# Performance work log

Measured on AMD Instinct MI355X. Metric: run time of the kernel, lower is better.

## Reference

```python
import jax, jax.numpy as jnp
import numpy as np

B, C, H, W = 16, 256, 56, 56
PH, PW = 7, 7            # partition (window) size
HEADS, DH = 8, 32        # n_heads = C // head_dim
P = PH * PW              # tokens per window = 49
GH, GW = H // PH, W // PW
G = GH * GW              # number of windows = 64
MLP = 4                  # mlp_ratio
EPS = 1e-5
SCALE = C ** (-0.5)      # note: torch code scales by feat_dim, not head_dim


def _rel_index(h, w):
    coords = np.stack(np.meshgrid(np.arange(h), np.arange(w), indexing='ij'))  # [2,h,w]
    cf = coords.reshape(2, -1)
    rel = cf[:, :, None] - cf[:, None, :]              # [2,P,P]
    rel = rel.transpose(1, 2, 0)
    rel[:, :, 0] += h - 1
    rel[:, :, 1] += w - 1
    rel[:, :, 0] *= 2 * w - 1
    return rel.sum(-1).astype(np.int32)                # [P,P]


def setup_inputs() -> dict:
    key = jax.random.key(0)
    ks = jax.random.split(key, 8)
    std = 0.02
    return {
        'x': jax.random.normal(ks[0], (B, C, H, W), jnp.float32),
        'ln1_g': jnp.ones((C,), jnp.float32),
        'ln1_b': jnp.zeros((C,), jnp.float32),
        'wqkv': jax.random.normal(ks[1], (C, 3 * C), jnp.float32) * std,
        'bqkv': jnp.zeros((3 * C,), jnp.float32),
        'wmerge': jax.random.normal(ks[2], (C, C), jnp.float32) * std,
        'bmerge': jnp.zeros((C,), jnp.float32),
        'bias_table': jax.random.normal(ks[3], ((2 * PH - 1) * (2 * PW - 1), HEADS), jnp.float32) * std,
        'ln2_g': jnp.ones((C,), jnp.float32),
        'ln2_b': jnp.zeros((C,), jnp.float32),
        'w1': jax.random.normal(ks[4], (C, MLP * C), jnp.float32) * std,
        'b1': jnp.zeros((MLP * C,), jnp.float32),
        'w2': jax.random.normal(ks[5], (MLP * C, C), jnp.float32) * std,
        'b2': jnp.zeros((C,), jnp.float32),
        'rel_idx': jnp.asarray(_rel_index(PH, PW)),
    }


def _layernorm(x, g, b):
    mu = jnp.mean(x, axis=-1, keepdims=True)
    var = jnp.var(x, axis=-1, keepdims=True)
    return (x - mu) * jax.lax.rsqrt(var + EPS) * g + b


def reference(x, ln1_g, ln1_b, wqkv, bqkv, wmerge, bmerge, bias_table,
              ln2_g, ln2_b, w1, b1, w2, b2, rel_idx):
    # --- window partition: [B,C,H,W] -> [B,G,P,C]
    xw = x.reshape(B, C, GH, PH, GW, PW).transpose(0, 2, 4, 3, 5, 1).reshape(B, G, P, C)

    # --- relative-position attention block
    y = _layernorm(xw, ln1_g, ln1_b)
    qkv = y @ wqkv + bqkv                               # [B,G,P,3C]
    q, k, v = jnp.split(qkv, 3, axis=-1)
    q = q.reshape(B, G, P, HEADS, DH)
    k = k.reshape(B, G, P, HEADS, DH) * SCALE
    v = v.reshape(B, G, P, HEADS, DH)
    scores = jnp.einsum('bgihd,bgjhd->bghij', q, k)     # [B,G,H,P,P]
    bias = bias_table[rel_idx].transpose(2, 0, 1)       # [H,P,P]
    attn = jax.nn.softmax(scores + bias[None, None], axis=-1)
    out = jnp.einsum('bghij,bgjhd->bgihd', attn, v).reshape(B, G, P, C)
    out = out @ wmerge + bmerge
    xw = xw + out

    # --- MLP block
    z = _layernorm(xw, ln2_g, ln2_b)
    z = jax.nn.gelu(z @ w1 + b1, approximate=False) @ w2 + b2
    xw = xw + z

    # --- window departition: [B,G,P,C] -> [B,C,H,W]
    xo = xw.reshape(B, GH, GW, PH, PW, C).transpose(0, 5, 1, 3, 2, 4).reshape(B, C, H, W)
    return xo
```

## Files before the change

### kernel.cpp

```cpp
#include <hip/hip_runtime.h>
#include <hip/hip_bf16.h>

#define B_      16
#define C_      256
#define H_      56
#define W_      56
#define HW_     3136
#define G_      64
#define P_      49
#define NTOK    50176
#define HEADS_  8
#define DH_     32
#define SCALE_  0.0625f
#define EPS_    1e-5f

typedef short bf16x8 __attribute__((ext_vector_type(8)));
typedef short bf16x4_t __attribute__((ext_vector_type(4)));
typedef float f32x4  __attribute__((ext_vector_type(4)));
using bf16 = __hip_bfloat16;

__device__ __forceinline__ void gload16(const void* g, void* l) {
  __builtin_amdgcn_global_load_lds((const __attribute__((address_space(1))) void*)g,
                                   (__attribute__((address_space(3))) void*)l, 16, 0, 0);
}
__device__ __forceinline__ float b2f(short s) {
  union { float f; unsigned u; } v; v.u = ((unsigned)(unsigned short)s) << 16; return v.f;
}
__device__ __forceinline__ short f2b(float f) {
  union { float f; unsigned u; } v; v.f = f;
  unsigned r = (v.u + 0x7FFFu + ((v.u >> 16) & 1u)) >> 16;
  return (short)r;
}

__global__ __launch_bounds__(256)
void prep_kernel(const float* __restrict__ wqkv, const float* __restrict__ wmerge,
                 const float* __restrict__ w1, const float* __restrict__ w2,
                 const float* __restrict__ btab, const int* __restrict__ relidx,
                 bf16* __restrict__ wqkvT, bf16* __restrict__ wmergeT,
                 bf16* __restrict__ w1T, bf16* __restrict__ w2T,
                 short* __restrict__ bt)
{
  int idx = blockIdx.x * 256 + threadIdx.x;
  if (idx < 196608) { int n = idx >> 8, k = idx & 255;
    wqkvT[idx] = __float2bfloat16(wqkv[k * 768 + n]); return; }
  idx -= 196608;
  if (idx < 65536) { int n = idx >> 8, k = idx & 255;
    wmergeT[idx] = __float2bfloat16(wmerge[k * 256 + n]); return; }
  idx -= 65536;
  if (idx < 262144) { int n = idx >> 8, k = idx & 255;
    w1T[idx] = __float2bfloat16(w1[k * 1024 + n]); return; }
  idx -= 262144;
  if (idx < 262144) { int n = idx >> 10, k = idx & 1023;
    w2T[idx] = __float2bfloat16(w2[k * 256 + n]); return; }
  idx -= 262144;
  if (idx < 32768) {
    int h = idx >> 12, rest = idx & 4095;
    int key = rest >> 6, col = rest & 63;
    int q = col >> 2, qni = col & 3;
    int query = qni * 16 + q;
    float v = 0.f;
    if (key < P_ && query < P_) v = btab[relidx[query * P_ + key] * HEADS_ + h];
    bt[idx] = f2b(v);
  }
}

__global__ __launch_bounds__(256)
void ingest_kernel(const float* __restrict__ x, const float* __restrict__ gam,
                   const float* __restrict__ bet, short* __restrict__ xtok,
                   short* __restrict__ y)
{
  __shared__ short Lt[56 * 260];
  const int h = blockIdx.x % 56, b = blockIdx.x / 56;
  const int tid = threadIdx.x;

  const float* xb = x + (size_t)b * 256 * HW_ + h * 56;
#pragma unroll
  for (int i = 0; i < 14; i++) {
    int idx = i * 256 + tid;
    int c = idx / 14, w4 = idx - c * 14;
    float4 v = *(const float4*)(xb + (size_t)c * HW_ + w4 * 4);
    Lt[(w4 * 4 + 0) * 260 + c] = f2b(v.x);
    Lt[(w4 * 4 + 1) * 260 + c] = f2b(v.y);
    Lt[(w4 * 4 + 2) * 260 + c] = f2b(v.z);
    Lt[(w4 * 4 + 3) * 260 + c] = f2b(v.w);
  }
  __syncthreads();

  const int lane = tid & 63, wv = tid >> 6;
  float4 gv = *(const float4*)(gam + lane * 4);
  float4 bv = *(const float4*)(bet + lane * 4);
  const int hdiv = h / 7, hmod = h - hdiv * 7;

  for (int t = 0; t < 14; t++) {
    int w = wv * 14 + t;
    bf16x4_t raw = *(const bf16x4_t*)&Lt[w * 260 + lane * 4];
    float f0 = b2f(raw[0]), f1 = b2f(raw[1]), f2 = b2f(raw[2]), f3 = b2f(raw[3]);
    float sum = f0 + f1 + f2 + f3;
    float sq  = f0*f0 + f1*f1 + f2*f2 + f3*f3;
#pragma unroll
    for (int off = 32; off > 0; off >>= 1) {
      sum += __shfl_xor(sum, off, 64);
      sq  += __shfl_xor(sq,  off, 64);
    }
    float mu = sum * (1.0f / 256.0f);
    float var = sq * (1.0f / 256.0f) - mu * mu;
    float rs = rsqrtf(var + EPS_);
    int wdiv = w / 7, wmod = w - wdiv * 7;
    int tok = b * HW_ + (hdiv * 8 + wdiv) * P_ + hmod * 7 + wmod;
    *(bf16x4_t*)(xtok + (size_t)tok * 256 + lane * 4) = raw;
    bf16x4_t o;
    o[0] = f2b((f0 - mu) * rs * gv.x + bv.x);
    o[1] = f2b((f1 - mu) * rs * gv.y + bv.y);
    o[2] = f2b((f2 - mu) * rs * gv.z + bv.z);
    o[3] = f2b((f3 - mu) * rs * gv.w + bv.w);
    *(bf16x4_t*)(y + (size_t)tok * 256 + lane * 4) = o;
  }
}

__global__ __launch_bounds__(256)
void ln2_kernel(const short* __restrict__ xw, const float* __restrict__ gam,
                const float* __restrict__ bet, short* __restrict__ z)
{
  const int t = blockIdx.x * 4 + (threadIdx.x >> 6);
  const int lane = threadIdx.x & 63;
  bf16x4_t raw = *(const bf16x4_t*)(xw + (size_t)t * 256 + lane * 4);
  float v[4];
#pragma unroll
  for (int j = 0; j < 4; j++) v[j] = b2f(raw[j]);
  float sum = v[0] + v[1] + v[2] + v[3];
  float sq  = v[0]*v[0] + v[1]*v[1] + v[2]*v[2] + v[3]*v[3];
#pragma unroll
  for (int off = 32; off > 0; off >>= 1) {
    sum += __shfl_xor(sum, off, 64);
    sq  += __shfl_xor(sq,  off, 64);
  }
  float mu = sum * (1.0f / 256.0f);
  float var = sq * (1.0f / 256.0f) - mu * mu;
  float rs = rsqrtf(var + EPS_);
  bf16x4_t o;
#pragma unroll
  for (int j = 0; j < 4; j++) {
    int c = lane * 4 + j;
    o[j] = f2b((v[j] - mu) * rs * gam[c] + bet[c]);
  }
  *(bf16x4_t*)(z + (size_t)t * 256 + lane * 4) = o;
}

__global__ __launch_bounds__(256)
void egress_kernel(const short* __restrict__ outtok, float* __restrict__ out)
{
  const int h = blockIdx.x % 56, b = blockIdx.x / 56;
  const int w = threadIdx.x & 63, cblk = threadIdx.x >> 6;
  const bool act = w < 56;
  const int wcl = act ? w : 55;
  const int tok = b * HW_ + ((h / 7) * 8 + wcl / 7) * P_ + (h % 7) * 7 + (wcl % 7);
  const short* src = outtok + (size_t)tok * 256 + cblk * 64;
  float* dst = out + ((size_t)b * 256 + cblk * 64) * HW_ + h * 56 + w;
#pragma unroll
  for (int j0 = 0; j0 < 64; j0 += 8) {
    bf16x8 r = *(const bf16x8*)(src + j0);
#pragma unroll
    for (int jj = 0; jj < 8; jj++)
      if (act) dst[(size_t)(j0 + jj) * HW_] = b2f(r[jj]);
  }
}

__global__ __launch_bounds__(64)
void attn_kernel(const short* __restrict__ qkv, const short* __restrict__ bt,
                 short* __restrict__ out)
{
  __shared__ short Pbuf[64 * 72];
  const int bid = blockIdx.x;
  const int h = bid & 7;
  const int t0 = (bid >> 3) * P_;
  const int lane = threadIdx.x;
  const int g = lane >> 4, q = lane & 15;

  const short* qb = qkv + (size_t)t0 * 768 + h * 32;

  bf16x8 vf[2][2];
#pragma unroll
  for (int kkt = 0; kkt < 2; kkt++)
#pragma unroll
    for (int n2 = 0; n2 < 2; n2++)
#pragma unroll
      for (int jj = 0; jj < 8; jj++) {
        int key = kkt * 32 + 8 * g + jj; key = key > 48 ? 48 : key;
        vf[kkt][n2][jj] = qb[(size_t)key * 768 + 512 + n2 * 16 + q];
      }

  bf16x8 kf[4], qf[4];
#pragma unroll
  for (int mi = 0; mi < 4; mi++) {
    int r_ = mi * 16 + q; r_ = r_ > 48 ? 48 : r_;
    kf[mi] = *(const bf16x8*)(qb + (size_t)r_ * 768 + 256 + 8 * g);
  }
#pragma unroll
  for (int ni = 0; ni < 4; ni++) {
    int r_ = ni * 16 + q; r_ = r_ > 48 ? 48 : r_;
    qf[ni] = *(const bf16x8*)(qb + (size_t)r_ * 768 + 8 * g);
  }

  f32x4 sacc[4][4] = {};
#pragma unroll
  for (int mi = 0; mi < 4; mi++)
#pragma unroll
    for (int ni = 0; ni < 4; ni++)
      sacc[mi][ni] = __builtin_amdgcn_mfma_f32_16x16x32_bf16(kf[mi], qf[ni], sacc[mi][ni], 0, 0, 0);

  float mx[4] = {-1e30f, -1e30f, -1e30f, -1e30f};
  const short* btb = bt + (size_t)(h * 64) * 64 + q * 4;
#pragma unroll
  for (int mi = 0; mi < 4; mi++)
#pragma unroll
    for (int r = 0; r < 4; r++) {
      int key = mi * 16 + 4 * g + r;
      bf16x4_t bv = *(const bf16x4_t*)(btb + key * 64);
      bool valid = key < P_;
#pragma unroll
      for (int ni = 0; ni < 4; ni++) {
        float s = valid ? fmaf(sacc[mi][ni][r], SCALE_, b2f(bv[ni])) : -1e30f;
        sacc[mi][ni][r] = s;
        mx[ni] = fmaxf(mx[ni], s);
      }
    }
#pragma unroll
  for (int ni = 0; ni < 4; ni++) {
    mx[ni] = fmaxf(mx[ni], __shfl_xor(mx[ni], 16, 64));
    mx[ni] = fmaxf(mx[ni], __shfl_xor(mx[ni], 32, 64));
  }
  float sm[4] = {0.f, 0.f, 0.f, 0.f};
#pragma unroll
  for (int mi = 0; mi < 4; mi++)
#pragma unroll
    for (int ni = 0; ni < 4; ni++)
#pragma unroll
      for (int r = 0; r < 4; r++) {
        float p = __expf(sacc[mi][ni][r] - mx[ni]);
        sacc[mi][ni][r] = p;
        sm[ni] += p;
      }
#pragma unroll
  for (int ni = 0; ni < 4; ni++) {
    sm[ni] += __shfl_xor(sm[ni], 16, 64);
    sm[ni] += __shfl_xor(sm[ni], 32, 64);
    sm[ni] = 1.0f / sm[ni];
  }
#pragma unroll
  for (int ni = 0; ni < 4; ni++)
#pragma unroll
    for (int mi = 0; mi < 4; mi++) {
      bf16x4_t pv;
#pragma unroll
      for (int r = 0; r < 4; r++) pv[r] = f2b(sacc[mi][ni][r] * sm[ni]);
      *(bf16x4_t*)&Pbuf[(ni * 16 + q) * 72 + mi * 16 + 4 * g] = pv;
    }
  __syncthreads();

  f32x4 oacc[4][2] = {};
#pragma unroll
  for (int kkt = 0; kkt < 2; kkt++) {
    bf16x8 paf[4];
#pragma unroll
    for (int qi = 0; qi < 4; qi++)
      paf[qi] = *(const bf16x8*)&Pbuf[(qi * 16 + q) * 72 + kkt * 32 + 8 * g];
#pragma unroll
    for (int qi = 0; qi < 4; qi++)
#pragma unroll
      for (int n2 = 0; n2 < 2; n2++)
        oacc[qi][n2] = __builtin_amdgcn_mfma_f32_16x16x32_bf16(paf[qi], vf[kkt][n2], oacc[qi][n2], 0, 0, 0);
  }

  short* ob = out + (size_t)t0 * 256 + h * 32;
#pragma unroll
  for (int qi = 0; qi < 4; qi++)
#pragma unroll
    for (int r = 0; r < 4; r++) {
      int query = qi * 16 + 4 * g + r;
      if (query < P_) {
#pragma unroll
        for (int n2 = 0; n2 < 2; n2++)
          ob[(size_t)query * 256 + n2 * 16 + q] = f2b(oacc[qi][n2][r]);
      }
    }
}

template<int EPI, int WN>
__global__ __launch_bounds__(128 * WN)
void gemm_kernel(const bf16* __restrict__ A, const bf16* __restrict__ Wt,
                 const float* __restrict__ bias, int N, int K,
                 bf16* __restrict__ outb, short* __restrict__ res_io)
{
  constexpr int THREADS = 128 * WN;
  constexpr int BN = 64 * WN;
  constexpr int RPP = THREADS / 4;
  constexpr int APASS = 128 / RPP;
  constexpr int BPASS = BN / RPP;
  constexpr int NLOADS = APASS + BPASS;
  __shared__ __align__(16) bf16 As[2][128 * 32];
  __shared__ __align__(16) bf16 Bs[2][BN * 32];

  const int tid = threadIdx.x;
  const int lane = tid & 63;
  const int wave = tid >> 6;
  const int wr = wave / WN, wc = wave % WN;
  const int bm = blockIdx.y * 128, bn = blockIdx.x * BN;

  f32x4 acc[4][4] = {};

  const int trow = tid >> 2;
  const int tcol = ((tid & 3) ^ ((tid >> 3) & 3)) * 8;
  const bf16* aA[APASS];
#pragma unroll
  for (int p = 0; p < APASS; p++)
    aA[p] = A + (size_t)(bm + p * RPP + trow) * K + tcol;
  const bf16* aB[BPASS];
#pragma unroll
  for (int p = 0; p < BPASS; p++)
    aB[p] = Wt + (size_t)(bn + p * RPP + trow) * K + tcol;
  const int dOff = tid * 8;

  const int kc_sw = ((lane >> 4) ^ ((lane >> 1) & 3)) * 8;
  const int l15 = lane & 15, g = lane >> 4;
  const int rA = wr * 64 + l15;
  const int rB = wc * 64 + l15;

  const int nt = K >> 5;

#pragma unroll
  for (int p = 0; p < APASS; p++) gload16(aA[p], &As[0][p * RPP * 32 + dOff]);
#pragma unroll
  for (int p = 0; p < BPASS; p++) gload16(aB[p], &Bs[0][p * RPP * 32 + dOff]);
#pragma unroll
  for (int p = 0; p < APASS; p++) gload16(aA[p] + 32, &As[1][p * RPP * 32 + dOff]);
#pragma unroll
  for (int p = 0; p < BPASS; p++) gload16(aB[p] + 32, &Bs[1][p * RPP * 32 + dOff]);

  for (int t = 0; t < nt; ++t) {
    const int cur = t & 1;
    if (t + 1 < nt) {
      if constexpr (NLOADS == 3) asm volatile("s_waitcnt vmcnt(3)" ::: "memory");
      else                       asm volatile("s_waitcnt vmcnt(4)" ::: "memory");
    } else {
      asm volatile("s_waitcnt vmcnt(0)" ::: "memory");
    }
    __builtin_amdgcn_s_barrier();

    bf16x8 af[4], bfr[4];
#pragma unroll
    for (int i = 0; i < 4; i++) {
      af[i]  = *(const bf16x8*)(&As[cur][(rA + i * 16) * 32 + kc_sw]);
      bfr[i] = *(const bf16x8*)(&Bs[cur][(rB + i * 16) * 32 + kc_sw]);
    }
#pragma unroll
    for (int mi = 0; mi < 4; mi++)
#pragma unroll
      for (int ni = 0; ni < 4; ni++)
        acc[mi][ni] = __builtin_amdgcn_mfma_f32_16x16x32_bf16(af[mi], bfr[ni], acc[mi][ni], 0, 0, 0);

    __builtin_amdgcn_s_barrier();
    if (t + 2 < nt) {
      const int k2 = (t + 2) << 5;
#pragma unroll
      for (int p = 0; p < APASS; p++) gload16(aA[p] + k2, &As[cur][p * RPP * 32 + dOff]);
#pragma unroll
      for (int p = 0; p < BPASS; p++) gload16(aB[p] + k2, &Bs[cur][p * RPP * 32 + dOff]);
    }
  }

#pragma unroll
  for (int mi = 0; mi < 4; mi++) {
#pragma unroll
    for (int ni = 0; ni < 4; ni++) {
#pragma unroll
      for (int r = 0; r < 4; r++) {
        const int row = bm + wr * 64 + mi * 16 + g * 4 + r;
        const int col = bn + wc * 64 + ni * 16 + l15;
        float v = acc[mi][ni][r] + bias[col];
        if (EPI == 0) {
          outb[(size_t)row * N + col] = __float2bfloat16(v);
        } else if (EPI == 1) {
          float gv = 0.5f * v * (1.0f + erff(v * 0.70710678118f));
          outb[(size_t)row * N + col] = __float2bfloat16(gv);
        } else {
          size_t o = (size_t)row * 256 + col;
          res_io[o] = f2b(v + b2f(res_io[o]));
        }
      }
    }
  }
}

extern "C" void kernel_launch(void* const* d_in, const int* in_sizes, int n_in,
                              void* d_out, int out_size, void* d_ws, size_t ws_size,
                              hipStream_t stream)
{
  const float* x      = (const float*)d_in[0];
  const float* ln1_g  = (const float*)d_in[1];
  const float* ln1_b  = (const float*)d_in[2];
  const float* wqkv   = (const float*)d_in[3];
  const float* bqkv   = (const float*)d_in[4];
  const float* wmerge = (const float*)d_in[5];
  const float* bmerge = (const float*)d_in[6];
  const float* btab   = (const float*)d_in[7];
  const float* ln2_g  = (const float*)d_in[8];
  const float* ln2_b  = (const float*)d_in[9];
  const float* w1     = (const float*)d_in[10];
  const float* b1     = (const float*)d_in[11];
  const float* w2     = (const float*)d_in[12];
  const float* b2     = (const float*)d_in[13];
  const int*   relidx = (const int*)d_in[14];
  float* out = (float*)d_out;

  char* ws = (char*)d_ws;
  bf16*  wqkvT   = (bf16*)(ws);
  bf16*  wmergeT = (bf16*)(ws + 393216);
  bf16*  w1T     = (bf16*)(ws + 524288);
  bf16*  w2T     = (bf16*)(ws + 1048576);
  short* battn   = (short*)(ws + 1572864);
  short* R1      = (short*)(ws + 1638400);
  short* R2      = (short*)(ws + 27328512);
  short* qkvc    = (short*)(ws + 53018624);
  short* attnc   = (short*)(ws + 91553792);
  short* hbuf    = (short*)(ws + 53018624);

  prep_kernel<<<3200, 256, 0, stream>>>(wqkv, wmerge, w1, w2, btab, relidx,
                                        wqkvT, wmergeT, w1T, w2T, battn);

  ingest_kernel<<<896, 256, 0, stream>>>(x, ln1_g, ln1_b, R1, R2);

  for (int c = 0; c < 2; ++c) {
    size_t r0 = (size_t)c * 25088;
    gemm_kernel<0, 4><<<dim3(3, 196), 512, 0, stream>>>(
        (const bf16*)(R2 + r0 * 256), wqkvT, bqkv, 768, 256, (bf16*)qkvc, nullptr);
    attn_kernel<<<4096, 64, 0, stream>>>(qkvc, battn, attnc);
    gemm_kernel<2, 2><<<dim3(2, 196), 256, 0, stream>>>(
        (const bf16*)attnc, wmergeT, bmerge, 256, 256, nullptr, R1 + r0 * 256);
  }

  ln2_kernel<<<NTOK / 4, 256, 0, stream>>>(R1, ln2_g, ln2_b, R2);

  for (int c = 0; c < 2; ++c) {
    size_t r0 = (size_t)c * 25088;
    gemm_kernel<1, 4><<<dim3(4, 196), 512, 0, stream>>>(
        (const bf16*)(R2 + r0 * 256), w1T, b1, 1024, 256, (bf16*)hbuf, nullptr);
    gemm_kernel<2, 2><<<dim3(2, 196), 256, 0, stream>>>(
        (const bf16*)hbuf, w2T, b2, 256, 1024, nullptr, R1 + r0 * 256);
  }

  egress_kernel<<<896, 256, 0, stream>>>(R1, out);
}
```

Baseline: 284.4 us.

## Fold LayerNorm into QKV and MLP1 GEMM epilogues via per-token stats

The LayerNorm gains are folded into the transposed weights, and per-column vectors u (gamma·W) and vb (beta·W + bias) are precomputed in the prep kernel. The ingest and ln2 kernels now write only per-token (mean, rstd) instead of a full normalized bf16 activation tensor. The GEMMs consume the raw residual and apply rstd*(acc - mean*u) + vb in the epilogue. This removes a write and a read of two 25 MB activation tensors. In exchange it loses some precision: the GEMM runs on un-centered bf16 inputs, which risks cancellation, and the prep kernel gains serial 256-step dot-product loops.

Measured after the change: 301.1 us. 1.06x slower.

```diff
diff --git a/kernel.cpp b/kernel.cpp
--- a/kernel.cpp
+++ b/kernel.cpp
@@ -36,19 +36,24 @@
 void prep_kernel(const float* __restrict__ wqkv, const float* __restrict__ wmerge,
                  const float* __restrict__ w1, const float* __restrict__ w2,
                  const float* __restrict__ btab, const int* __restrict__ relidx,
+                 const float* __restrict__ g1, const float* __restrict__ bln1,
+                 const float* __restrict__ g2, const float* __restrict__ bln2,
+                 const float* __restrict__ bqkv, const float* __restrict__ b1,
                  bf16* __restrict__ wqkvT, bf16* __restrict__ wmergeT,
                  bf16* __restrict__ w1T, bf16* __restrict__ w2T,
-                 short* __restrict__ bt)
+                 short* __restrict__ bt,
+                 float* __restrict__ u1, float* __restrict__ vb1,
+                 float* __restrict__ u2, float* __restrict__ vb2)
 {
   int idx = blockIdx.x * 256 + threadIdx.x;
   if (idx < 196608) { int n = idx >> 8, k = idx & 255;
-    wqkvT[idx] = __float2bfloat16(wqkv[k * 768 + n]); return; }
+    wqkvT[idx] = __float2bfloat16(wqkv[k * 768 + n] * g1[k]); return; }
   idx -= 196608;
   if (idx < 65536) { int n = idx >> 8, k = idx & 255;
     wmergeT[idx] = __float2bfloat16(wmerge[k * 256 + n]); return; }
   idx -= 65536;
   if (idx < 262144) { int n = idx >> 8, k = idx & 255;
-    w1T[idx] = __float2bfloat16(w1[k * 1024 + n]); return; }
+    w1T[idx] = __float2bfloat16(w1[k * 1024 + n] * g2[k]); return; }
   idx -= 262144;
   if (idx < 262144) { int n = idx >> 10, k = idx & 1023;
     w2T[idx] = __float2bfloat16(w2[k * 256 + n]); return; }
@@ -61,13 +66,34 @@
     float v = 0.f;
     if (key < P_ && query < P_) v = btab[relidx[query * P_ + key] * HEADS_ + h];
     bt[idx] = f2b(v);
+    return;
+  }
+  idx -= 32768;
+  if (idx < 768) {
+    float u = 0.f, vb = bqkv[idx];
+    for (int k = 0; k < 256; ++k) {
+      float w = wqkv[k * 768 + idx];
+      u  += g1[k]  * w;
+      vb += bln1[k] * w;
+    }
+    u1[idx] = u; vb1[idx] = vb;
+    return;
+  }
+  idx -= 768;
+  if (idx < 1024) {
+    float u = 0.f, vb = b1[idx];
+    for (int k = 0; k < 256; ++k) {
+      float w = w1[k * 1024 + idx];
+      u  += g2[k]  * w;
+      vb += bln2[k] * w;
+    }
+    u2[idx] = u; vb2[idx] = vb;
   }
 }
 
 __global__ __launch_bounds__(256)
-void ingest_kernel(const float* __restrict__ x, const float* __restrict__ gam,
-                   const float* __restrict__ bet, short* __restrict__ xtok,
-                   short* __restrict__ y)
+void ingest_kernel(const float* __restrict__ x, short* __restrict__ xtok,
+                   float2* __restrict__ stats)
 {
   __shared__ short Lt[56 * 260];
   const int h = blockIdx.x % 56, b = blockIdx.x / 56;
@@ -87,8 +113,6 @@
   __syncthreads();
 
   const int lane = tid & 63, wv = tid >> 6;
-  float4 gv = *(const float4*)(gam + lane * 4);
-  float4 bv = *(const float4*)(bet + lane * 4);
   const int hdiv = h / 7, hmod = h - hdiv * 7;
 
   for (int t = 0; t < 14; t++) {
@@ -108,27 +132,19 @@
     int wdiv = w / 7, wmod = w - wdiv * 7;
     int tok = b * HW_ + (hdiv * 8 + wdiv) * P_ + hmod * 7 + wmod;
     *(bf16x4_t*)(xtok + (size_t)tok * 256 + lane * 4) = raw;
-    bf16x4_t o;
-    o[0] = f2b((f0 - mu) * rs * gv.x + bv.x);
-    o[1] = f2b((f1 - mu) * rs * gv.y + bv.y);
-    o[2] = f2b((f2 - mu) * rs * gv.z + bv.z);
-    o[3] = f2b((f3 - mu) * rs * gv.w + bv.w);
-    *(bf16x4_t*)(y + (size_t)tok * 256 + lane * 4) = o;
+    if (lane == 0) stats[tok] = make_float2(mu, rs);
   }
 }
 
 __global__ __launch_bounds__(256)
-void ln2_kernel(const short* __restrict__ xw, const float* __restrict__ gam,
-                const float* __restrict__ bet, short* __restrict__ z)
+void ln2stats_kernel(const short* __restrict__ xw, float2* __restrict__ stats)
 {
   const int t = blockIdx.x * 4 + (threadIdx.x >> 6);
   const int lane = threadIdx.x & 63;
   bf16x4_t raw = *(const bf16x4_t*)(xw + (size_t)t * 256 + lane * 4);
-  float v[4];
-#pragma unroll
-  for (int j = 0; j < 4; j++) v[j] = b2f(raw[j]);
-  float sum = v[0] + v[1] + v[2] + v[3];
-  float sq  = v[0]*v[0] + v[1]*v[1] + v[2]*v[2] + v[3]*v[3];
+  float v0 = b2f(raw[0]), v1 = b2f(raw[1]), v2 = b2f(raw[2]), v3 = b2f(raw[3]);
+  float sum = v0 + v1 + v2 + v3;
+  float sq  = v0*v0 + v1*v1 + v2*v2 + v3*v3;
 #pragma unroll
   for (int off = 32; off > 0; off >>= 1) {
     sum += __shfl_xor(sum, off, 64);
@@ -137,13 +153,7 @@
   float mu = sum * (1.0f / 256.0f);
   float var = sq * (1.0f / 256.0f) - mu * mu;
   float rs = rsqrtf(var + EPS_);
-  bf16x4_t o;
-#pragma unroll
-  for (int j = 0; j < 4; j++) {
-    int c = lane * 4 + j;
-    o[j] = f2b((v[j] - mu) * rs * gam[c] + bet[c]);
-  }
-  *(bf16x4_t*)(z + (size_t)t * 256 + lane * 4) = o;
+  if (lane == 0) stats[t] = make_float2(mu, rs);
 }
 
 __global__ __launch_bounds__(256)
@@ -289,7 +299,9 @@
 __global__ __launch_bounds__(128 * WN)
 void gemm_kernel(const bf16* __restrict__ A, const bf16* __restrict__ Wt,
                  const float* __restrict__ bias, int N, int K,
-                 bf16* __restrict__ outb, short* __restrict__ res_io)
+                 bf16* __restrict__ outb, short* __restrict__ res_io,
+                 const float2* __restrict__ stats,
+                 const float* __restrict__ uvec, const float* __restrict__ vbvec)
 {
   constexpr int THREADS = 128 * WN;
   constexpr int BN = 64 * WN;
@@ -366,6 +378,33 @@
 #pragma unroll
       for (int p = 0; p < BPASS; p++) gload16(aB[p] + k2, &Bs[cur][p * RPP * 32 + dOff]);
     }
+  }
+
+  if constexpr (EPI == 4 || EPI == 5) {
+    float uj[4], vbj[4];
+#pragma unroll
+    for (int ni = 0; ni < 4; ni++) {
+      const int col = bn + wc * 64 + ni * 16 + l15;
+      uj[ni]  = uvec[col];
+      vbj[ni] = vbvec[col];
+    }
+#pragma unroll
+    for (int mi = 0; mi < 4; mi++) {
+#pragma unroll
+      for (int r = 0; r < 4; r++) {
+        const int row = bm + wr * 64 + mi * 16 + g * 4 + r;
+        float2 s = stats[row];
+        float a = s.y, cmu = s.y * s.x;
+#pragma unroll
+        for (int ni = 0; ni < 4; ni++) {
+          const int col = bn + wc * 64 + ni * 16 + l15;
+          float v = fmaf(a, acc[mi][ni][r], fmaf(-cmu, uj[ni], vbj[ni]));
+          if (EPI == 5) v = 0.5f * v * (1.0f + erff(v * 0.70710678118f));
+          outb[(size_t)row * N + col] = __float2bfloat16(v);
+        }
+      }
+    }
+    return;
   }
 
 #pragma unroll
@@ -413,39 +452,50 @@
   float* out = (float*)d_out;
 
   char* ws = (char*)d_ws;
-  bf16*  wqkvT   = (bf16*)(ws);
-  bf16*  wmergeT = (bf16*)(ws + 393216);
-  bf16*  w1T     = (bf16*)(ws + 524288);
-  bf16*  w2T     = (bf16*)(ws + 1048576);
-  short* battn   = (short*)(ws + 1572864);
-  short* R1      = (short*)(ws + 1638400);
-  short* R2      = (short*)(ws + 27328512);
-  short* qkvc    = (short*)(ws + 53018624);
-  short* attnc   = (short*)(ws + 91553792);
-  short* hbuf    = (short*)(ws + 53018624);
-
-  prep_kernel<<<3200, 256, 0, stream>>>(wqkv, wmerge, w1, w2, btab, relidx,
-                                        wqkvT, wmergeT, w1T, w2T, battn);
-
-  ingest_kernel<<<896, 256, 0, stream>>>(x, ln1_g, ln1_b, R1, R2);
+  bf16*   wqkvT   = (bf16*)(ws);
+  bf16*   wmergeT = (bf16*)(ws + 393216);
+  bf16*   w1T     = (bf16*)(ws + 524288);
+  bf16*   w2T     = (bf16*)(ws + 1048576);
+  short*  battn   = (short*)(ws + 1572864);
+  float*  u1      = (float*)(ws + 1638400);
+  float*  vb1     = (float*)(ws + 1641472);
+  float*  u2      = (float*)(ws + 1644544);
+  float*  vb2     = (float*)(ws + 1648640);
+  float2* stats1  = (float2*)(ws + 1652736);
+  float2* stats2  = (float2*)(ws + 2054144);
+  short*  R1      = (short*)(ws + 2455552);
+  short*  qkvc    = (short*)(ws + 28145664);
+  short*  attnc   = (short*)(ws + 66680832);
+  short*  hbuf    = (short*)(ws + 28145664);
+
+  prep_kernel<<<3207, 256, 0, stream>>>(wqkv, wmerge, w1, w2, btab, relidx,
+                                        ln1_g, ln1_b, ln2_g, ln2_b, bqkv, b1,
+                                        wqkvT, wmergeT, w1T, w2T, battn,
+                                        u1, vb1, u2, vb2);
+
+  ingest_kernel<<<896, 256, 0, stream>>>(x, R1, stats1);
 
   for (int c = 0; c < 2; ++c) {
     size_t r0 = (size_t)c * 25088;
-    gemm_kernel<0, 4><<<dim3(3, 196), 512, 0, stream>>>(
-        (const bf16*)(R2 + r0 * 256), wqkvT, bqkv, 768, 256, (bf16*)qkvc, nullptr);
+    gemm_kernel<4, 4><<<dim3(3, 196), 512, 0, stream>>>(
+        (const bf16*)(R1 + r0 * 256), wqkvT, nullptr, 768, 256, (bf16*)qkvc,
+        nullptr, stats1 + r0, u1, vb1);
     attn_kernel<<<4096, 64, 0, stream>>>(qkvc, battn, attnc);
     gemm_kernel<2, 2><<<dim3(2, 196), 256, 0, stream>>>(
-        (const bf16*)attnc, wmergeT, bmerge, 256, 256, nullptr, R1 + r0 * 256);
-  }
-
-  ln2_kernel<<<NTOK / 4, 256, 0, stream>>>(R1, ln2_g, ln2_b, R2);
+        (const bf16*)attnc, wmergeT, bmerge, 256, 256, nullptr, R1 + r0 * 256,
+        nullptr, nullptr, nullptr);
+  }
+
+  ln2stats_kernel<<<NTOK / 4, 256, 0, stream>>>(R1, stats2);
 
   for (int c = 0; c < 2; ++c) {
     size_t r0 = (size_t)c * 25088;
-    gemm_kernel<1, 4><<<dim3(4, 196), 512, 0, stream>>>(
-        (const bf16*)(R2 + r0 * 256), w1T, b1, 1024, 256, (bf16*)hbuf, nullptr);
+    gemm_kernel<5, 4><<<dim3(4, 196), 512, 0, stream>>>(
+        (const bf16*)(R1 + r0 * 256), w1T, nullptr, 1024, 256, (bf16*)hbuf,
+        nullptr, stats2 + r0, u2, vb2);
     gemm_kernel<2, 2><<<dim3(2, 196), 256, 0, stream>>>(
-        (const bf16*)hbuf, w2T, b2, 256, 1024, nullptr, R1 + r0 * 256);
+        (const bf16*)hbuf, w2T, b2, 256, 1024, nullptr, R1 + r0 * 256,
+        nullptr, nullptr, nullptr);
   }
 
   egress_kernel<<<896, 256, 0, stream>>>(R1, out);
```

## Use 256x256 GEMM tiles for wide GEMMs and single-chunk execution when workspace allows

Applied to the files above, without the earlier changes.

The GEMM template is generalized over warp rows, warp columns and N-fragments per warp. The QKV and FC1 GEMMs now use 256x256 block tiles (8 MFMA N-fragments per wave), which raises data reuse from LDS and reduces global loads per FLOP. The bias load is hoisted out of the inner loop. The host code also runs a single token chunk instead of two whenever the workspace is large enough, removing half the launches and enlarging each grid. In exchange, the accumulators need more registers, and the wide GEMMs have fewer, larger blocks, which can hurt wave-count balance across CUs.

New measurement: 304.3 us. +7.0%, slower.

```diff
diff --git a/kernel.cpp b/kernel.cpp
--- a/kernel.cpp
+++ b/kernel.cpp
@@ -285,28 +285,28 @@
     }
 }
 
-template<int EPI, int WN>
-__global__ __launch_bounds__(128 * WN)
+template<int EPI, int WR, int WC, int NI>
+__global__ __launch_bounds__(WR * WC * 64)
 void gemm_kernel(const bf16* __restrict__ A, const bf16* __restrict__ Wt,
                  const float* __restrict__ bias, int N, int K,
                  bf16* __restrict__ outb, short* __restrict__ res_io)
 {
-  constexpr int THREADS = 128 * WN;
-  constexpr int BN = 64 * WN;
+  constexpr int THREADS = WR * WC * 64;
+  constexpr int BM = WR * 64;
+  constexpr int BN = WC * NI * 16;
   constexpr int RPP = THREADS / 4;
-  constexpr int APASS = 128 / RPP;
+  constexpr int APASS = BM / RPP;
   constexpr int BPASS = BN / RPP;
-  constexpr int NLOADS = APASS + BPASS;
-  __shared__ __align__(16) bf16 As[2][128 * 32];
+  __shared__ __align__(16) bf16 As[2][BM * 32];
   __shared__ __align__(16) bf16 Bs[2][BN * 32];
 
   const int tid = threadIdx.x;
   const int lane = tid & 63;
   const int wave = tid >> 6;
-  const int wr = wave / WN, wc = wave % WN;
-  const int bm = blockIdx.y * 128, bn = blockIdx.x * BN;
-
-  f32x4 acc[4][4] = {};
+  const int wr = wave / WC, wc = wave % WC;
+  const int bm = blockIdx.y * BM, bn = blockIdx.x * BN;
+
+  f32x4 acc[4][NI] = {};
 
   const int trow = tid >> 2;
   const int tcol = ((tid & 3) ^ ((tid >> 3) & 3)) * 8;
@@ -323,7 +323,7 @@
   const int kc_sw = ((lane >> 4) ^ ((lane >> 1) & 3)) * 8;
   const int l15 = lane & 15, g = lane >> 4;
   const int rA = wr * 64 + l15;
-  const int rB = wc * 64 + l15;
+  const int rB = wc * (NI * 16) + l15;
 
   const int nt = K >> 5;
 
@@ -338,24 +338,21 @@
 
   for (int t = 0; t < nt; ++t) {
     const int cur = t & 1;
-    if (t + 1 < nt) {
-      if constexpr (NLOADS == 3) asm volatile("s_waitcnt vmcnt(3)" ::: "memory");
-      else                       asm volatile("s_waitcnt vmcnt(4)" ::: "memory");
-    } else {
-      asm volatile("s_waitcnt vmcnt(0)" ::: "memory");
-    }
+    if (t + 1 < nt) asm volatile("s_waitcnt vmcnt(4)" ::: "memory");
+    else            asm volatile("s_waitcnt vmcnt(0)" ::: "memory");
     __builtin_amdgcn_s_barrier();
 
-    bf16x8 af[4], bfr[4];
-#pragma unroll
-    for (int i = 0; i < 4; i++) {
+    bf16x8 af[4], bfr[NI];
+#pragma unroll
+    for (int i = 0; i < 4; i++)
       af[i]  = *(const bf16x8*)(&As[cur][(rA + i * 16) * 32 + kc_sw]);
+#pragma unroll
+    for (int i = 0; i < NI; i++)
       bfr[i] = *(const bf16x8*)(&Bs[cur][(rB + i * 16) * 32 + kc_sw]);
-    }
 #pragma unroll
     for (int mi = 0; mi < 4; mi++)
 #pragma unroll
-      for (int ni = 0; ni < 4; ni++)
+      for (int ni = 0; ni < NI; ni++)
         acc[mi][ni] = __builtin_amdgcn_mfma_f32_16x16x32_bf16(af[mi], bfr[ni], acc[mi][ni], 0, 0, 0);
 
     __builtin_amdgcn_s_barrier();
@@ -371,12 +368,13 @@
 #pragma unroll
   for (int mi = 0; mi < 4; mi++) {
 #pragma unroll
-    for (int ni = 0; ni < 4; ni++) {
+    for (int ni = 0; ni < NI; ni++) {
+      const int col = bn + wc * (NI * 16) + ni * 16 + l15;
+      const float bv = bias[col];
 #pragma unroll
       for (int r = 0; r < 4; r++) {
         const int row = bm + wr * 64 + mi * 16 + g * 4 + r;
-        const int col = bn + wc * 64 + ni * 16 + l15;
-        float v = acc[mi][ni][r] + bias[col];
+        float v = acc[mi][ni][r] + bv;
         if (EPI == 0) {
           outb[(size_t)row * N + col] = __float2bfloat16(v);
         } else if (EPI == 1) {
@@ -420,31 +418,34 @@
   short* battn   = (short*)(ws + 1572864);
   short* R1      = (short*)(ws + 1638400);
   short* R2      = (short*)(ws + 27328512);
-  short* qkvc    = (short*)(ws + 53018624);
-  short* attnc   = (short*)(ws + 91553792);
-  short* hbuf    = (short*)(ws + 53018624);
+  const size_t CH1_NEED = 53018624ull + (size_t)NTOK * 1024 * 2 + (size_t)NTOK * 256 * 2;
+  const int nchunk = (ws_size >= CH1_NEED) ? 1 : 2;
+  const int ctok = NTOK / nchunk;
+  short* qkvc  = (short*)(ws + 53018624);
+  short* attnc = qkvc + (size_t)ctok * 768;
+  short* hbuf  = qkvc;
 
   prep_kernel<<<3200, 256, 0, stream>>>(wqkv, wmerge, w1, w2, btab, relidx,
                                         wqkvT, wmergeT, w1T, w2T, battn);
 
   ingest_kernel<<<896, 256, 0, stream>>>(x, ln1_g, ln1_b, R1, R2);
 
-  for (int c = 0; c < 2; ++c) {
-    size_t r0 = (size_t)c * 25088;
-    gemm_kernel<0, 4><<<dim3(3, 196), 512, 0, stream>>>(
+  for (int c = 0; c < nchunk; ++c) {
+    size_t r0 = (size_t)c * ctok;
+    gemm_kernel<0, 4, 2, 8><<<dim3(3, ctok / 256), 512, 0, stream>>>(
         (const bf16*)(R2 + r0 * 256), wqkvT, bqkv, 768, 256, (bf16*)qkvc, nullptr);
-    attn_kernel<<<4096, 64, 0, stream>>>(qkvc, battn, attnc);
-    gemm_kernel<2, 2><<<dim3(2, 196), 256, 0, stream>>>(
+    attn_kernel<<<(ctok / P_) * 8, 64, 0, stream>>>(qkvc, battn, attnc);
+    gemm_kernel<2, 2, 2, 4><<<dim3(2, ctok / 128), 256, 0, stream>>>(
         (const bf16*)attnc, wmergeT, bmerge, 256, 256, nullptr, R1 + r0 * 256);
   }
 
   ln2_kernel<<<NTOK / 4, 256, 0, stream>>>(R1, ln2_g, ln2_b, R2);
 
-  for (int c = 0; c < 2; ++c) {
-    size_t r0 = (size_t)c * 25088;
-    gemm_kernel<1, 4><<<dim3(4, 196), 512, 0, stream>>>(
+  for (int c = 0; c < nchunk; ++c) {
+    size_t r0 = (size_t)c * ctok;
+    gemm_kernel<1, 4, 2, 8><<<dim3(4, ctok / 256), 512, 0, stream>>>(
         (const bf16*)(R2 + r0 * 256), w1T, b1, 1024, 256, (bf16*)hbuf, nullptr);
-    gemm_kernel<2, 2><<<dim3(2, 196), 256, 0, stream>>>(
+    gemm_kernel<2, 2, 2, 4><<<dim3(2, ctok / 128), 256, 0, stream>>>(
         (const bf16*)hbuf, w2T, b2, 256, 1024, nullptr, R1 + r0 * 256);
   }
 
```
